# Kernel tuning notes

Hardware: AMD Instinct MI355X
Metric: run time of the kernel (lower is better)

The kernel has to match this reference:

```python
import jax, jax.numpy as jnp
import numpy as np

N_FILTER = 64
IMAGE_SIZE = 64
CHANNELS = 3
N_CALLS = 16  # n_calls * 16 with n_calls=1
EPS = 1e-5


def _sobel_kernels(c):
    kx = jnp.array([[-1., 0., 1.], [-2., 0., 2.], [-1., 0., 1.]], jnp.float32) / 8.0
    ky = kx.T
    # depthwise OIHW kernels: (C, 1, 3, 3)
    return jnp.tile(kx[None, None], (c, 1, 1, 1)), jnp.tile(ky[None, None], (c, 1, 1, 1))


def _dwconv(x, k):
    return jax.lax.conv_general_dilated(
        x, k, window_strides=(1, 1), padding='SAME',
        feature_group_count=x.shape[1],
        dimension_numbers=('NCHW', 'OIHW', 'NCHW'))


def setup_inputs() -> dict:
    key = jax.random.key(0)
    k1, k2, k3 = jax.random.split(key, 3)
    B, L = 16, 512
    fin, fout = N_FILTER * 3, N_FILTER
    return {
        'lat': jax.random.normal(k1, (B, L), jnp.float32),
        'Wk': jax.random.normal(k2, (L, fin * fout), jnp.float32) * 0.02,
        'bk': jnp.zeros((fin * fout,), jnp.float32),
        'Wb': jax.random.normal(k3, (L, fout), jnp.float32) * 0.02,
        'bb': jnp.zeros((fout,), jnp.float32),
        'leak_factor': jnp.asarray(0.1, jnp.float32),
    }


def reference(lat, Wk, bk, Wb, bb, leak_factor):
    B = lat.shape[0]
    fin, fout = N_FILTER * 3, N_FILTER
    kx, ky = _sobel_kernels(N_FILTER)

    # seed: zeros with a 1.0 in channel 0 at the image center
    out0 = jnp.zeros((B, N_FILTER, IMAGE_SIZE, IMAGE_SIZE), jnp.float32)
    out0 = out0.at[:, 0, IMAGE_SIZE // 2, IMAGE_SIZE // 2].set(1.0)

    leak = jnp.clip(leak_factor, 0.001, 1000.0)

    # per-sample dynamic 1x1 conv weights/bias (constant across the loop)
    w = (lat @ Wk + bk).reshape(B, fout, fin)   # (B, fout, fin)
    b = (lat @ Wb + bb)                          # (B, fout)

    def step(out, _):
        # Sobel perception: [identity, grad_x, grad_y] -> (B, 3*nf, H, W)
        p = jnp.concatenate([out, _dwconv(out, kx), _dwconv(out, ky)], axis=1)
        # InstanceNorm2d (affine=False): normalize over H, W per sample/channel
        mu = p.mean(axis=(2, 3), keepdims=True)
        var = p.var(axis=(2, 3), keepdims=True)
        p = (p - mu) * jax.lax.rsqrt(var + EPS)
        # latent-conditioned dynamic 1x1 conv
        new = jnp.einsum('bchw,boc->bohw', p, w) + b[:, :, None, None]
        out = out + leak * new
        return out, out

    out, embs = jax.lax.scan(step, out0, None, length=N_CALLS)
    out_embs = jnp.concatenate([out0[None], embs], axis=0)  # (N_CALLS+1, B, nf, H, W)

    out_raw = out[:, :CHANNELS]
    return jnp.clip(out_raw, -1.0, 1.0), out_embs, out_raw
```

## Files before the change

### kernel.cpp

```cpp
#include <hip/hip_runtime.h>
#include <cstdint>
#include <cstddef>

#define NB 16
#define NC 64
#define HW 4096
#define SLICE ((size_t)(NB*NC*HW))
#define NSTEP 16

#define WS_WT    ((size_t)0)
#define WS_BV    ((size_t)196608)
#define WS_LATT  ((size_t)197632)
#define WS_SV    ((size_t)205824)
#define WS_SVMU  ((size_t)208896)

typedef _Float16 half8 __attribute__((ext_vector_type(8)));
typedef float f32x4 __attribute__((ext_vector_type(4)));

__global__ void k_latT(const float* __restrict__ lat, float* __restrict__ latT) {
  int t = threadIdx.x;
  for (int idx = t; idx < 16*512; idx += 256) {
    int b = idx >> 9, k = idx & 511;
    latT[k*16 + b] = lat[idx];
  }
}

__global__ __launch_bounds__(256) void k_w(const float* __restrict__ latT,
    const float* __restrict__ Wk, const float* __restrict__ bk,
    const float* __restrict__ Wb, const float* __restrict__ bb,
    float* __restrict__ wT, float* __restrict__ bvec) {
  int t = threadIdx.x;
  if (blockIdx.x < 48) {
    int j = blockIdx.x*256 + t;
    float acc[16];
#pragma unroll
    for (int b = 0; b < 16; b++) acc[b] = 0.f;
#pragma unroll 4
    for (int k = 0; k < 512; k++) {
      float wv = Wk[(size_t)k*12288 + j];
      const float* lt = (const float*)__builtin_assume_aligned(latT + k*16, 64);
#pragma unroll
      for (int b = 0; b < 16; b++) acc[b] = fmaf(lt[b], wv, acc[b]);
    }
    int o = j / 192, cf = j % 192;
    int g = cf >> 6, c = cf & 63;
    float bkj = bk[j];
#pragma unroll
    for (int b = 0; b < 16; b++)
      wT[(((size_t)(b*3 + g))*64 + o)*64 + c] = acc[b] + bkj;
  } else if (t < 64) {
    int j = t;
    float acc[16];
#pragma unroll
    for (int b = 0; b < 16; b++) acc[b] = 0.f;
    for (int k = 0; k < 512; k++) {
      float wv = Wb[k*64 + j];
      const float* lt = (const float*)__builtin_assume_aligned(latT + k*16, 64);
#pragma unroll
      for (int b = 0; b < 16; b++) acc[b] = fmaf(lt[b], wv, acc[b]);
    }
    float bbj = bb[j];
#pragma unroll
    for (int b = 0; b < 16; b++) bvec[b*64 + j] = acc[b] + bbj;
  }
}

__global__ void k_init(float* __restrict__ e0) {
  int idx4 = (blockIdx.x*256 + threadIdx.x) * 4;
  float4 v = make_float4(0.f, 0.f, 0.f, 0.f);
  if ((idx4 & 262143) == 2080) v.x = 1.0f;
  *(float4*)(e0 + idx4) = v;
}

__global__ __launch_bounds__(256) void k_stats(const float* __restrict__ st,
    float* __restrict__ svb, float* __restrict__ svmub) {
  int c = blockIdx.x, b = blockIdx.y, t = threadIdx.x;
  __shared__ float img[HW];
  __shared__ float red[4][6];
  const size_t chan = (size_t)(b*NC + c) * HW;
  const float4* src4 = (const float4*)(st + chan);
  float4* img4 = (float4*)img;
#pragma unroll
  for (int i = 0; i < 4; i++) img4[i*256 + t] = src4[i*256 + t];
  __syncthreads();
  float s0=0,q0=0,s1=0,q1=0,s2=0,q2=0;
#pragma unroll
  for (int i = 0; i < 4; i++) {
    int base = i*1024 + t*4;
    int h = base >> 6, w0 = base & 63;
#pragma unroll
    for (int jj = 0; jj < 4; jj++) {
      int w = w0 + jj;
      bool wl = (w > 0), wr = (w < 63), hu = (h > 0), hd = (h < 63);
      float a00 = (hu && wl) ? img[(h-1)*64 + (w-1)] : 0.f;
      float a01 =  hu        ? img[(h-1)*64 +  w   ] : 0.f;
      float a02 = (hu && wr) ? img[(h-1)*64 + (w+1)] : 0.f;
      float a10 =  wl        ? img[ h   *64 + (w-1)] : 0.f;
      float a12 =  wr        ? img[ h   *64 + (w+1)] : 0.f;
      float a20 = (hd && wl) ? img[(h+1)*64 + (w-1)] : 0.f;
      float a21 =  hd        ? img[(h+1)*64 +  w   ] : 0.f;
      float a22 = (hd && wr) ? img[(h+1)*64 + (w+1)] : 0.f;
      float v = img[h*64 + w];
      float gx = (a02 - a00 + 2.f*(a12 - a10) + a22 - a20) * 0.125f;
      float gy = (a20 - a00 + 2.f*(a21 - a01) + a22 - a02) * 0.125f;
      s0 += v;  q0 = fmaf(v, v, q0);
      s1 += gx; q1 = fmaf(gx, gx, q1);
      s2 += gy; q2 = fmaf(gy, gy, q2);
    }
  }
#pragma unroll
  for (int off = 32; off >= 1; off >>= 1) {
    s0 += __shfl_xor(s0, off); q0 += __shfl_xor(q0, off);
    s1 += __shfl_xor(s1, off); q1 += __shfl_xor(q1, off);
    s2 += __shfl_xor(s2, off); q2 += __shfl_xor(q2, off);
  }
  int lane = t & 63, wv = t >> 6;
  if (lane == 0) {
    red[wv][0]=s0; red[wv][1]=q0; red[wv][2]=s1;
    red[wv][3]=q1; red[wv][4]=s2; red[wv][5]=q2;
  }
  __syncthreads();
  if (t == 0) {
    float r[6];
#pragma unroll
    for (int u = 0; u < 6; u++) r[u] = red[0][u]+red[1][u]+red[2][u]+red[3][u];
#pragma unroll
    for (int g = 0; g < 3; g++) {
      float mu  = r[2*g] * (1.f/HW);
      float var = fmaxf(r[2*g+1]*(1.f/HW) - mu*mu, 0.f);
      float sv  = 1.f / sqrtf(var + 1e-5f);
      svb  [b*192 + g*64 + c] = sv;
      svmub[b*192 + g*64 + c] = sv * mu;
    }
  }
}

__global__ __launch_bounds__(256, 2) void k_fused(const float* __restrict__ st,
    float* __restrict__ stn, const float* __restrict__ wT,
    const float* __restrict__ bvec, const float* __restrict__ svb,
    const float* __restrict__ svmub, const float* __restrict__ leakp) {
  int r = blockIdx.x, b = blockIdx.y, t = threadIdx.x;
  __shared__ __align__(16) float rawL[32*200];
  __shared__ __align__(16) _Float16 Bhi[4*192*8];
  __shared__ __align__(16) _Float16 Blo[4*192*8];
  __shared__ __align__(16) _Float16 Whi[3*64*32];
  __shared__ __align__(16) _Float16 Wlo[3*64*32];
  __shared__ float svL[192], svmuL[192], biasL[192], bvecL[64];

  if (t < 192) { svL[t] = svb[b*192 + t]; svmuL[t] = svmub[b*192 + t]; }
  if (t < 64) bvecL[t] = bvec[b*64 + t];
  float leak = fminf(fmaxf(leakp[0], 0.001f), 1000.f);

  int lane = t & 63;
  int wt = t >> 6;
  const float* stb = st + (size_t)b*NC*HW;
  float biasacc = 0.f;
  f32x4 accA[4] = {}; f32x4 accB[12] = {}; f32x4 accC[12] = {};

  for (int kc = 0; kc < 2; kc++) {
    __syncthreads();
#pragma unroll
    for (int i = 0; i < 6; i++) {
      int u = t + i*256;
      int c_rel = u / 48, q = u % 48;
      int rho = q >> 4, quad = q & 15;
      int row = r - 1 + rho;
      float4 v = make_float4(0.f,0.f,0.f,0.f);
      if (row >= 0 && row < 64)
        v = *(const float4*)(stb + (size_t)(kc*32 + c_rel)*HW + row*64 + quad*4);
      *(float4*)(rawL + c_rel*200 + rho*64 + quad*4) = v;
    }
    if (t < 192) {
      int g = t >> 6, o = t & 63;
      const float* wrow = wT + (((size_t)(b*3 + g))*64 + o)*64 + kc*32;
#pragma unroll
      for (int s = 0; s < 4; s++) {
        float4 va = *(const float4*)(wrow + s*8);
        float4 vb = *(const float4*)(wrow + s*8 + 4);
        float wv[8] = {va.x,va.y,va.z,va.w,vb.x,vb.y,vb.z,vb.w};
        half8 hv, lv;
#pragma unroll
        for (int jj = 0; jj < 8; jj++) {
          int cg = g*64 + kc*32 + s*8 + jj;
          float scaled = wv[jj] * svL[cg];
          biasacc = fmaf(wv[jj], svmuL[cg], biasacc);
          _Float16 h = (_Float16)scaled;
          hv[jj] = h;
          lv[jj] = (_Float16)(scaled - (float)h);
        }
        int sidx = (g*64 + o)*32 + ((s ^ (o & 3)) << 3);
        *(half8*)(Whi + sidx) = hv;
        *(half8*)(Wlo + sidx) = lv;
      }
    }
    __syncthreads();
#pragma unroll
    for (int i = 0; i < 3; i++) {
      int v = t + i*256;
      int c8 = v / 192, px = v % 192;
      half8 hv, lv;
#pragma unroll
      for (int ii = 0; ii < 8; ii++) {
        float x = rawL[(c8*8 + ii)*200 + px];
        _Float16 h = (_Float16)x;
        hv[ii] = h;
        lv[ii] = (_Float16)(x - (float)h);
      }
      *(half8*)(Bhi + (c8*192 + px)*8) = hv;
      *(half8*)(Blo + (c8*192 + px)*8) = lv;
    }
    __syncthreads();
    half8 ahi[3], alo[3];
#pragma unroll
    for (int g = 0; g < 3; g++) {
      int oa = wt*16 + (lane & 15);
      int sidx = (g*64 + oa)*32 + (((lane >> 4) ^ (oa & 3)) << 3);
      ahi[g] = *(const half8*)(Whi + sidx);
      alo[g] = *(const half8*)(Wlo + sidx);
    }
#pragma unroll
    for (int n = 0; n < 12; n++) {
      int bidx = ((lane >> 4)*192 + n*16 + (lane & 15))*8;
      half8 bh = *(const half8*)(Bhi + bidx);
      half8 bl = *(const half8*)(Blo + bidx);
      accB[n] = __builtin_amdgcn_mfma_f32_16x16x32_f16(ahi[1], bh, accB[n], 0,0,0);
      accB[n] = __builtin_amdgcn_mfma_f32_16x16x32_f16(ahi[1], bl, accB[n], 0,0,0);
      accB[n] = __builtin_amdgcn_mfma_f32_16x16x32_f16(alo[1], bh, accB[n], 0,0,0);
      accC[n] = __builtin_amdgcn_mfma_f32_16x16x32_f16(ahi[2], bh, accC[n], 0,0,0);
      accC[n] = __builtin_amdgcn_mfma_f32_16x16x32_f16(ahi[2], bl, accC[n], 0,0,0);
      accC[n] = __builtin_amdgcn_mfma_f32_16x16x32_f16(alo[2], bh, accC[n], 0,0,0);
      if (n >= 4 && n < 8) {
        accA[n-4] = __builtin_amdgcn_mfma_f32_16x16x32_f16(ahi[0], bh, accA[n-4], 0,0,0);
        accA[n-4] = __builtin_amdgcn_mfma_f32_16x16x32_f16(ahi[0], bl, accA[n-4], 0,0,0);
        accA[n-4] = __builtin_amdgcn_mfma_f32_16x16x32_f16(alo[0], bh, accA[n-4], 0,0,0);
      }
    }
  }

  if (t < 192) biasL[t] = biasacc;
  __syncthreads();

#pragma unroll
  for (int j = 0; j < 4; j++) {
    int o = wt*16 + ((lane >> 4) << 2) + j;
    float Sx[4], Sy[4];
#pragma unroll
    for (int nc = 0; nc < 4; nc++) {
      Sx[nc] = accB[nc][j] + 2.f*accB[4+nc][j] + accB[8+nc][j];
      Sy[nc] = accC[8+nc][j] - accC[nc][j];
    }
    float bt = bvecL[o] - biasL[o] - biasL[64+o] - biasL[128+o];
#pragma unroll
    for (int nc = 0; nc < 4; nc++) {
      int nm = (nc > 0) ? nc-1 : 0;
      int np = (nc < 3) ? nc+1 : 3;
      float xl1 = __shfl(Sx[nc], (lane - 1) & 63);
      float xl2 = (nc > 0) ? __shfl(Sx[nm], (lane + 15) & 63) : 0.f;
      float xL  = (lane & 15) ? xl1 : xl2;
      float xr1 = __shfl(Sx[nc], (lane + 1) & 63);
      float xr2 = (nc < 3) ? __shfl(Sx[np], (lane - 15) & 63) : 0.f;
      float xR  = ((lane & 15) == 15) ? xr2 : xr1;
      float yl1 = __shfl(Sy[nc], (lane - 1) & 63);
      float yl2 = (nc > 0) ? __shfl(Sy[nm], (lane + 15) & 63) : 0.f;
      float yL  = (lane & 15) ? yl1 : yl2;
      float yr1 = __shfl(Sy[nc], (lane + 1) & 63);
      float yr2 = (nc < 3) ? __shfl(Sy[np], (lane - 15) & 63) : 0.f;
      float yR  = ((lane & 15) == 15) ? yr2 : yr1;
      float gx = (xR - xL) * 0.125f;
      float gy = (yL + 2.f*Sy[nc] + yR) * 0.125f;
      float nw = accA[nc][j] + gx + gy + bt;
      int w = nc*16 + (lane & 15);
      size_t gi = (size_t)(b*NC + o)*HW + (size_t)r*64 + w;
      stn[gi] = st[gi] + leak * nw;
    }
  }
}

__global__ void k_final(const float* __restrict__ stF, float* __restrict__ out0,
                        float* __restrict__ out2) {
  int i4 = (blockIdx.x*256 + threadIdx.x)*4;
  int b = i4 / 12288, rr = i4 % 12288;
  float4 v = *(const float4*)(stF + (size_t)b*(NC*HW) + rr);
  float4 cv;
  cv.x = fminf(fmaxf(v.x,-1.f),1.f);
  cv.y = fminf(fmaxf(v.y,-1.f),1.f);
  cv.z = fminf(fmaxf(v.z,-1.f),1.f);
  cv.w = fminf(fmaxf(v.w,-1.f),1.f);
  *(float4*)(out0 + i4) = cv;
  *(float4*)(out2 + i4) = v;
}

extern "C" void kernel_launch(void* const* d_in, const int* in_sizes, int n_in,
                              void* d_out, int out_size, void* d_ws, size_t ws_size,
                              hipStream_t stream) {
  const float* lat   = (const float*)d_in[0];
  const float* Wk    = (const float*)d_in[1];
  const float* bk    = (const float*)d_in[2];
  const float* Wb    = (const float*)d_in[3];
  const float* bb    = (const float*)d_in[4];
  const float* leakp = (const float*)d_in[5];
  float* out = (float*)d_out;
  float* ws  = (float*)d_ws;
  float* wT    = ws + WS_WT;
  float* bvec  = ws + WS_BV;
  float* latT  = ws + WS_LATT;
  float* svbuf = ws + WS_SV;
  float* svmub = ws + WS_SVMU;
  float* out0 = out;
  float* embs = out + 196608;
  float* out2 = out + 196608 + 17*SLICE;

  hipLaunchKernelGGL(k_latT, dim3(1),    dim3(256), 0, stream, lat, latT);
  hipLaunchKernelGGL(k_w,    dim3(49),   dim3(256), 0, stream, latT, Wk, bk, Wb, bb, wT, bvec);
  hipLaunchKernelGGL(k_init, dim3(4096), dim3(256), 0, stream, embs);
  for (int tstep = 0; tstep < NSTEP; tstep++) {
    const float* stc = embs + (size_t)tstep*SLICE;
    float*       stn = embs + (size_t)(tstep+1)*SLICE;
    hipLaunchKernelGGL(k_stats, dim3(64,16), dim3(256), 0, stream, stc, svbuf, svmub);
    hipLaunchKernelGGL(k_fused, dim3(64,16), dim3(256), 0, stream,
                       stc, stn, wT, bvec, svbuf, svmub, leakp);
  }
  hipLaunchKernelGGL(k_final, dim3(192), dim3(256), 0, stream,
                     embs + (size_t)NSTEP*SLICE, out0, out2);
}
```

Baseline: 730.2 us.

## Fuse all steps into one persistent cooperative kernel with grid barriers

Replaces the 32 per-step stats/fused launches plus the init and final kernels with a single cooperative kernel of 256 blocks of 512 threads. Each block runs two 256-thread groups and separates the stats and update phases with a hand-written atomic grid barrier. The weight scaling and split-half conversion move into a per-step prelude that both groups share. This removes launch gaps and tail effects. In exchange it brings grid-barrier latency, lower parallelism (256 blocks versus 1024), larger shared memory use, and the risk of deadlock if not all blocks are co-resident.

```diff
diff --git a/kernel.cpp b/kernel.cpp
--- a/kernel.cpp
+++ b/kernel.cpp
@@ -7,18 +7,36 @@
 #define HW 4096
 #define SLICE ((size_t)(NB*NC*HW))
 #define NSTEP 16
+#define GRIDB 256
 
 #define WS_WT    ((size_t)0)
 #define WS_BV    ((size_t)196608)
 #define WS_LATT  ((size_t)197632)
 #define WS_SV    ((size_t)205824)
 #define WS_SVMU  ((size_t)208896)
+#define WS_BAR   ((size_t)211968)
 
 typedef _Float16 half8 __attribute__((ext_vector_type(8)));
 typedef float f32x4 __attribute__((ext_vector_type(4)));
 
-__global__ void k_latT(const float* __restrict__ lat, float* __restrict__ latT) {
+struct SharedA2 {
+  float img[2][4096];
+  float red[2][4][6];
+};
+struct SharedB2 {
+  alignas(16) float rawL[2][6400];
+  alignas(16) _Float16 Bhi[2][6144];
+  alignas(16) _Float16 Blo[2][6144];
+  alignas(16) _Float16 Whi[12288];
+  alignas(16) _Float16 Wlo[12288];
+  float svL[192], svmuL[192], biasL[192], bvecL[64];
+};
+union SharedU { SharedA2 a; SharedB2 b; };
+
+__global__ void k_latT(const float* __restrict__ lat, float* __restrict__ latT,
+                       unsigned* __restrict__ bar) {
   int t = threadIdx.x;
+  if (t == 0) { bar[0] = 0u; bar[1] = 0u; }
   for (int idx = t; idx < 16*512; idx += 256) {
     int b = idx >> 9, k = idx & 511;
     latT[k*16 + b] = lat[idx];
@@ -65,28 +83,40 @@
   }
 }
 
-__global__ void k_init(float* __restrict__ e0) {
-  int idx4 = (blockIdx.x*256 + threadIdx.x) * 4;
-  float4 v = make_float4(0.f, 0.f, 0.f, 0.f);
-  if ((idx4 & 262143) == 2080) v.x = 1.0f;
-  *(float4*)(e0 + idx4) = v;
-}
-
-__global__ __launch_bounds__(256) void k_stats(const float* __restrict__ st,
-    float* __restrict__ svb, float* __restrict__ svmub) {
-  int c = blockIdx.x, b = blockIdx.y, t = threadIdx.x;
-  __shared__ float img[HW];
-  __shared__ float red[4][6];
+__device__ __forceinline__ void gridbar(unsigned* bar) {
+  __syncthreads();
+  if (threadIdx.x == 0) {
+    __threadfence();
+    unsigned g = __hip_atomic_load(&bar[1], __ATOMIC_RELAXED, __HIP_MEMORY_SCOPE_AGENT);
+    unsigned v = __hip_atomic_fetch_add(&bar[0], 1u, __ATOMIC_ACQ_REL, __HIP_MEMORY_SCOPE_AGENT);
+    if (v == (unsigned)(GRIDB - 1)) {
+      __hip_atomic_store(&bar[0], 0u, __ATOMIC_RELAXED, __HIP_MEMORY_SCOPE_AGENT);
+      __hip_atomic_fetch_add(&bar[1], 1u, __ATOMIC_RELEASE, __HIP_MEMORY_SCOPE_AGENT);
+    } else {
+      while (__hip_atomic_load(&bar[1], __ATOMIC_ACQUIRE, __HIP_MEMORY_SCOPE_AGENT) == g)
+        __builtin_amdgcn_s_sleep(1);
+    }
+    __threadfence();
+  }
+  __syncthreads();
+}
+
+__device__ void phaseA2(SharedU& sh, int grp, int t8, int vb,
+                        const float* __restrict__ st,
+                        float* __restrict__ svb, float* __restrict__ svmub) {
+  int c = vb & 63, b = vb >> 6;
+  __syncthreads();
   const size_t chan = (size_t)(b*NC + c) * HW;
   const float4* src4 = (const float4*)(st + chan);
-  float4* img4 = (float4*)img;
-#pragma unroll
-  for (int i = 0; i < 4; i++) img4[i*256 + t] = src4[i*256 + t];
-  __syncthreads();
+  float4* img4 = (float4*)sh.a.img[grp];
+#pragma unroll
+  for (int i = 0; i < 4; i++) img4[i*256 + t8] = src4[i*256 + t8];
+  __syncthreads();
+  const float* img = sh.a.img[grp];
   float s0=0,q0=0,s1=0,q1=0,s2=0,q2=0;
 #pragma unroll
   for (int i = 0; i < 4; i++) {
-    int base = i*1024 + t*4;
+    int base = i*1024 + t8*4;
     int h = base >> 6, w0 = base & 63;
 #pragma unroll
     for (int jj = 0; jj < 4; jj++) {
@@ -114,16 +144,17 @@
     s1 += __shfl_xor(s1, off); q1 += __shfl_xor(q1, off);
     s2 += __shfl_xor(s2, off); q2 += __shfl_xor(q2, off);
   }
-  int lane = t & 63, wv = t >> 6;
+  int lane = t8 & 63, wv = t8 >> 6;
   if (lane == 0) {
-    red[wv][0]=s0; red[wv][1]=q0; red[wv][2]=s1;
-    red[wv][3]=q1; red[wv][4]=s2; red[wv][5]=q2;
-  }
-  __syncthreads();
-  if (t == 0) {
+    sh.a.red[grp][wv][0]=s0; sh.a.red[grp][wv][1]=q0; sh.a.red[grp][wv][2]=s1;
+    sh.a.red[grp][wv][3]=q1; sh.a.red[grp][wv][4]=s2; sh.a.red[grp][wv][5]=q2;
+  }
+  __syncthreads();
+  if (t8 == 0) {
     float r[6];
 #pragma unroll
-    for (int u = 0; u < 6; u++) r[u] = red[0][u]+red[1][u]+red[2][u]+red[3][u];
+    for (int u = 0; u < 6; u++)
+      r[u] = sh.a.red[grp][0][u]+sh.a.red[grp][1][u]+sh.a.red[grp][2][u]+sh.a.red[grp][3][u];
 #pragma unroll
     for (int g = 0; g < 3; g++) {
       float mu  = r[2*g] * (1.f/HW);
@@ -135,94 +166,95 @@
   }
 }
 
-__global__ __launch_bounds__(256, 2) void k_fused(const float* __restrict__ st,
-    float* __restrict__ stn, const float* __restrict__ wT,
-    const float* __restrict__ bvec, const float* __restrict__ svb,
-    const float* __restrict__ svmub, const float* __restrict__ leakp) {
-  int r = blockIdx.x, b = blockIdx.y, t = threadIdx.x;
-  __shared__ __align__(16) float rawL[32*200];
-  __shared__ __align__(16) _Float16 Bhi[4*192*8];
-  __shared__ __align__(16) _Float16 Blo[4*192*8];
-  __shared__ __align__(16) _Float16 Whi[3*64*32];
-  __shared__ __align__(16) _Float16 Wlo[3*64*32];
-  __shared__ float svL[192], svmuL[192], biasL[192], bvecL[64];
-
-  if (t < 192) { svL[t] = svb[b*192 + t]; svmuL[t] = svmub[b*192 + t]; }
-  if (t < 64) bvecL[t] = bvec[b*64 + t];
-  float leak = fminf(fmaxf(leakp[0], 0.001f), 1000.f);
-
-  int lane = t & 63;
-  int wt = t >> 6;
+__device__ void stepB_prelude(SharedU& sh, int b, int t,
+    const float* __restrict__ wT, const float* __restrict__ bvec,
+    const float* __restrict__ svb, const float* __restrict__ svmub) {
+  __syncthreads();
+  if (t < 192) { sh.b.svL[t] = svb[b*192 + t]; sh.b.svmuL[t] = svmub[b*192 + t]; }
+  if (t < 64) sh.b.bvecL[t] = bvec[b*64 + t];
+  __syncthreads();
+  if (t < 192) {
+    int gso = t >> 6, o = t & 63;
+    float biasacc = 0.f;
+#pragma unroll
+    for (int kc = 0; kc < 2; kc++) {
+      const float* wrow = wT + (((size_t)(b*3 + gso))*64 + o)*64 + kc*32;
+#pragma unroll
+      for (int s = 0; s < 4; s++) {
+        float4 va = *(const float4*)(wrow + s*8);
+        float4 vb4 = *(const float4*)(wrow + s*8 + 4);
+        float wv[8] = {va.x,va.y,va.z,va.w,vb4.x,vb4.y,vb4.z,vb4.w};
+        half8 hv, lv;
+#pragma unroll
+        for (int jj = 0; jj < 8; jj++) {
+          int cg = gso*64 + kc*32 + s*8 + jj;
+          float scaled = wv[jj] * sh.b.svL[cg];
+          biasacc = fmaf(wv[jj], sh.b.svmuL[cg], biasacc);
+          _Float16 h = (_Float16)scaled;
+          hv[jj] = h;
+          lv[jj] = (_Float16)(scaled - (float)h);
+        }
+        int sidx = kc*6144 + (gso*64 + o)*32 + ((s ^ (o & 3)) << 3);
+        *(half8*)(sh.b.Whi + sidx) = hv;
+        *(half8*)(sh.b.Wlo + sidx) = lv;
+      }
+    }
+    sh.b.biasL[t] = biasacc;
+  }
+  __syncthreads();
+}
+
+__device__ void unitB(SharedU& sh, int grp, int t8, int b, int r,
+                      const float* __restrict__ st, float* __restrict__ stn,
+                      float leak) {
+  int lane = t8 & 63;
+  int wt = t8 >> 6;
   const float* stb = st + (size_t)b*NC*HW;
-  float biasacc = 0.f;
   f32x4 accA[4] = {}; f32x4 accB[12] = {}; f32x4 accC[12] = {};
 
   for (int kc = 0; kc < 2; kc++) {
     __syncthreads();
 #pragma unroll
     for (int i = 0; i < 6; i++) {
-      int u = t + i*256;
+      int u = t8 + i*256;
       int c_rel = u / 48, q = u % 48;
       int rho = q >> 4, quad = q & 15;
       int row = r - 1 + rho;
       float4 v = make_float4(0.f,0.f,0.f,0.f);
       if (row >= 0 && row < 64)
         v = *(const float4*)(stb + (size_t)(kc*32 + c_rel)*HW + row*64 + quad*4);
-      *(float4*)(rawL + c_rel*200 + rho*64 + quad*4) = v;
-    }
-    if (t < 192) {
-      int g = t >> 6, o = t & 63;
-      const float* wrow = wT + (((size_t)(b*3 + g))*64 + o)*64 + kc*32;
-#pragma unroll
-      for (int s = 0; s < 4; s++) {
-        float4 va = *(const float4*)(wrow + s*8);
-        float4 vb = *(const float4*)(wrow + s*8 + 4);
-        float wv[8] = {va.x,va.y,va.z,va.w,vb.x,vb.y,vb.z,vb.w};
-        half8 hv, lv;
-#pragma unroll
-        for (int jj = 0; jj < 8; jj++) {
-          int cg = g*64 + kc*32 + s*8 + jj;
-          float scaled = wv[jj] * svL[cg];
-          biasacc = fmaf(wv[jj], svmuL[cg], biasacc);
-          _Float16 h = (_Float16)scaled;
-          hv[jj] = h;
-          lv[jj] = (_Float16)(scaled - (float)h);
-        }
-        int sidx = (g*64 + o)*32 + ((s ^ (o & 3)) << 3);
-        *(half8*)(Whi + sidx) = hv;
-        *(half8*)(Wlo + sidx) = lv;
-      }
+      *(float4*)(sh.b.rawL[grp] + c_rel*200 + rho*64 + quad*4) = v;
     }
     __syncthreads();
 #pragma unroll
     for (int i = 0; i < 3; i++) {
-      int v = t + i*256;
+      int v = t8 + i*256;
       int c8 = v / 192, px = v % 192;
       half8 hv, lv;
 #pragma unroll
       for (int ii = 0; ii < 8; ii++) {
-        float x = rawL[(c8*8 + ii)*200 + px];
+        float x = sh.b.rawL[grp][(c8*8 + ii)*200 + px];
         _Float16 h = (_Float16)x;
         hv[ii] = h;
         lv[ii] = (_Float16)(x - (float)h);
       }
-      *(half8*)(Bhi + (c8*192 + px)*8) = hv;
-      *(half8*)(Blo + (c8*192 + px)*8) = lv;
+      *(half8*)(sh.b.Bhi[grp] + (c8*192 + px)*8) = hv;
+      *(half8*)(sh.b.Blo[grp] + (c8*192 + px)*8) = lv;
     }
     __syncthreads();
     half8 ahi[3], alo[3];
 #pragma unroll
-    for (int g = 0; g < 3; g++) {
+    for (int gso = 0; gso < 3; gso++) {
       int oa = wt*16 + (lane & 15);
-      int sidx = (g*64 + oa)*32 + (((lane >> 4) ^ (oa & 3)) << 3);
-      ahi[g] = *(const half8*)(Whi + sidx);
-      alo[g] = *(const half8*)(Wlo + sidx);
+      int sidx = kc*6144 + (gso*64 + oa)*32 + (((lane >> 4) ^ (oa & 3)) << 3);
+      ahi[gso] = *(const half8*)(sh.b.Whi + sidx);
+      alo[gso] = *(const half8*)(sh.b.Wlo + sidx);
     }
 #pragma unroll
     for (int n = 0; n < 12; n++) {
       int bidx = ((lane >> 4)*192 + n*16 + (lane & 15))*8;
-      half8 bh = *(const half8*)(Bhi + bidx);
-      half8 bl = *(const half8*)(Blo + bidx);
+      half8 bh = *(const half8*)(sh.b.Bhi[grp] + bidx);
+      half8 bl = *(const half8*)(sh.b.Blo[grp] + bidx);
       accB[n] = __builtin_amdgcn_mfma_f32_16x16x32_f16(ahi[1], bh, accB[n], 0,0,0);
       accB[n] = __builtin_amdgcn_mfma_f32_16x16x32_f16(ahi[1], bl, accB[n], 0,0,0);
       accB[n] = __builtin_amdgcn_mfma_f32_16x16x32_f16(alo[1], bh, accB[n], 0,0,0);
@@ -237,9 +269,6 @@
     }
   }
 
-  if (t < 192) biasL[t] = biasacc;
-  __syncthreads();
-
 #pragma unroll
   for (int j = 0; j < 4; j++) {
     int o = wt*16 + ((lane >> 4) << 2) + j;
@@ -249,7 +278,7 @@
       Sx[nc] = accB[nc][j] + 2.f*accB[4+nc][j] + accB[8+nc][j];
       Sy[nc] = accC[8+nc][j] - accC[nc][j];
     }
-    float bt = bvecL[o] - biasL[o] - biasL[64+o] - biasL[128+o];
+    float bt = sh.b.bvecL[o] - sh.b.biasL[o] - sh.b.biasL[64+o] - sh.b.biasL[128+o];
 #pragma unroll
     for (int nc = 0; nc < 4; nc++) {
       int nm = (nc > 0) ? nc-1 : 0;
@@ -276,18 +305,53 @@
   }
 }
 
-__global__ void k_final(const float* __restrict__ stF, float* __restrict__ out0,
-                        float* __restrict__ out2) {
-  int i4 = (blockIdx.x*256 + threadIdx.x)*4;
-  int b = i4 / 12288, rr = i4 % 12288;
-  float4 v = *(const float4*)(stF + (size_t)b*(NC*HW) + rr);
-  float4 cv;
-  cv.x = fminf(fmaxf(v.x,-1.f),1.f);
-  cv.y = fminf(fmaxf(v.y,-1.f),1.f);
-  cv.z = fminf(fmaxf(v.z,-1.f),1.f);
-  cv.w = fminf(fmaxf(v.w,-1.f),1.f);
-  *(float4*)(out0 + i4) = cv;
-  *(float4*)(out2 + i4) = v;
+__global__ __launch_bounds__(512, 2) void k_steps(float* __restrict__ embs,
+    const float* __restrict__ wT, const float* __restrict__ bvec,
+    float* __restrict__ svb, float* __restrict__ svmub,
+    const float* __restrict__ leakp, float* __restrict__ out0,
+    float* __restrict__ out2, unsigned* __restrict__ bar) {
+  __shared__ SharedU sh;
+  int bid = blockIdx.x, t = threadIdx.x;
+  int grp = t >> 8, t8 = t & 255;
+
+#pragma unroll
+  for (int i = 0; i < 8; i++) {
+    int u = bid*4096 + i*512 + t;
+    int idx4 = u*4;
+    float4 v = make_float4(0.f, 0.f, 0.f, 0.f);
+    if ((idx4 & 262143) == 2080) v.x = 1.0f;
+    *(float4*)(embs + idx4) = v;
+  }
+  gridbar(bar);
+
+  float leak = fminf(fmaxf(leakp[0], 0.001f), 1000.f);
+  int b = bid >> 4, r0 = bid & 15;
+  for (int step = 0; step < NSTEP; step++) {
+    const float* stc = embs + (size_t)step*SLICE;
+    float*       stn = embs + (size_t)(step+1)*SLICE;
+    phaseA2(sh, grp, t8, (bid<<2) | 0 | grp, stc, svb, svmub);
+    phaseA2(sh, grp, t8, (bid<<2) | 2 | grp, stc, svb, svmub);
+    gridbar(bar);
+    stepB_prelude(sh, b, t, wT, bvec, svb, svmub);
+    unitB(sh, grp, t8, b, r0 + (grp<<4),      stc, stn, leak);
+    unitB(sh, grp, t8, b, r0 + (grp<<4) + 32, stc, stn, leak);
+    gridbar(bar);
+  }
+
+  const float* stF = embs + (size_t)NSTEP*SLICE;
+  int u = bid*512 + t;
+  if (u < 49152) {
+    int i4 = u*4;
+    int bb2 = i4 / 12288, rr = i4 % 12288;
+    float4 v = *(const float4*)(stF + (size_t)bb2*(NC*HW) + rr);
+    float4 cv;
+    cv.x = fminf(fmaxf(v.x,-1.f),1.f);
+    cv.y = fminf(fmaxf(v.y,-1.f),1.f);
+    cv.z = fminf(fmaxf(v.z,-1.f),1.f);
+    cv.w = fminf(fmaxf(v.w,-1.f),1.f);
+    *(float4*)(out0 + i4) = cv;
+    *(float4*)(out2 + i4) = v;
+  }
 }
 
 extern "C" void kernel_launch(void* const* d_in, const int* in_sizes, int n_in,
@@ -306,20 +370,16 @@
   float* latT  = ws + WS_LATT;
   float* svbuf = ws + WS_SV;
   float* svmub = ws + WS_SVMU;
+  unsigned* bar = (unsigned*)(ws + WS_BAR);
   float* out0 = out;
   float* embs = out + 196608;
   float* out2 = out + 196608 + 17*SLICE;
 
-  hipLaunchKernelGGL(k_latT, dim3(1),    dim3(256), 0, stream, lat, latT);
-  hipLaunchKernelGGL(k_w,    dim3(49),   dim3(256), 0, stream, latT, Wk, bk, Wb, bb, wT, bvec);
-  hipLaunchKernelGGL(k_init, dim3(4096), dim3(256), 0, stream, embs);
-  for (int tstep = 0; tstep < NSTEP; tstep++) {
-    const float* stc = embs + (size_t)tstep*SLICE;
-    float*       stn = embs + (size_t)(tstep+1)*SLICE;
-    hipLaunchKernelGGL(k_stats, dim3(64,16), dim3(256), 0, stream, stc, svbuf, svmub);
-    hipLaunchKernelGGL(k_fused, dim3(64,16), dim3(256), 0, stream,
-                       stc, stn, wT, bvec, svbuf, svmub, leakp);
-  }
-  hipLaunchKernelGGL(k_final, dim3(192), dim3(256), 0, stream,
-                     embs + (size_t)NSTEP*SLICE, out0, out2);
-}
+  hipLaunchKernelGGL(k_latT, dim3(1),  dim3(256), 0, stream, lat, latT, bar);
+  hipLaunchKernelGGL(k_w,    dim3(49), dim3(256), 0, stream, latT, Wk, bk, Wb, bb, wT, bvec);
+
+  void* args[] = { &embs, &wT, &bvec, &svbuf, &svmub, (void*)&leakp,
+                   &out0, &out2, &bar };
+  hipLaunchCooperativeKernel((void*)k_steps, dim3(GRIDB), dim3(512),
+                             args, 0, stream);
+}
```

New measurement: 2.382 ms. 226% more time.
